# Kernel optimization log

Measured on AMD Instinct MI355X. Metric: run time of the kernel, lower is better.

The kernel has to match this reference:

```python
import jax, jax.numpy as jnp
import numpy as np

V, E, H = 100000, 128, 256
P1, P2 = 512, 128
B, S, F = 256, 200, 10


def setup_inputs() -> dict:
    key = jax.random.key(0)
    ks = jax.random.split(key, 12)
    s = lambda *d: 1.0 / np.sqrt(d[-1])
    inp = {
        "x": jax.random.randint(ks[0], (B, S, F), 0, V),
        "emb": jax.random.normal(ks[1], (V, E), jnp.float32) * 0.1,
        # PyTorch LSTM params: gates ordered (i, f, g, o), shapes [4H, E] / [4H, H]
        "W_ih": jax.random.normal(ks[2], (4 * H, E), jnp.float32) * s(E),
        "W_hh": jax.random.normal(ks[3], (4 * H, H), jnp.float32) * s(H),
        "b_ih": jax.random.normal(ks[4], (4 * H,), jnp.float32) * s(H),
        "b_hh": jax.random.normal(ks[5], (4 * H,), jnp.float32) * s(H),
        "W1": jax.random.normal(ks[6], (H, P1), jnp.float32) * s(H),
        "b1": jnp.zeros((P1,), jnp.float32),
        "W2": jax.random.normal(ks[7], (P1, P2), jnp.float32) * s(P1),
        "b2": jnp.zeros((P2,), jnp.float32),
        "W3": jax.random.normal(ks[8], (P2, 1), jnp.float32) * s(P2),
        "b3": jnp.zeros((1,), jnp.float32),
    }
    return inp


def reference(x, emb, W_ih, W_hh, b_ih, b_hh, W1, b1, W2, b2, W3, b3):
    # embedding + mean over field dim -> [B, S, E]
    e = jnp.take(emb, x, axis=0).mean(axis=-2)
    T = e.shape[1] // 2
    hist, tgt = e[:, :T], e[:, T:2 * T]
    b = e.shape[0]
    h0 = jnp.zeros((b, H), e.dtype)
    c0 = jnp.zeros((b, H), e.dtype)

    def lstm_step(carry, xt):
        h, c = carry
        g = xt @ W_ih.T + h @ W_hh.T + b_ih + b_hh  # [B, 4H]
        gi, gf, gg, go = jnp.split(g, 4, axis=-1)
        c = jax.nn.sigmoid(gf) * c + jax.nn.sigmoid(gi) * jnp.tanh(gg)
        h = jax.nn.sigmoid(go) * jnpp_tanh(c) if False else jax.nn.sigmoid(go) * jnp.tanh(c)
        return (h, c), None

    (hN, cN), _ = jax.lax.scan(lstm_step, (h0, c0), jnp.swapaxes(hist, 0, 1))

    # Each target step restarts from the SAME history state (loop reuses history_state),
    # so all T target steps are independent single LSTM steps -> fully batched.
    g = jnp.einsum('bte,ge->btg', tgt, W_ih) + (hN @ W_hh.T)[:, None, :] + b_ih + b_hh
    gi, gf, gg, go = jnp.split(g, 4, axis=-1)
    c = jax.nn.sigmoid(gf) * cN[:, None, :] + jax.nn.sigmoid(gi) * jnp.tanh(gg)
    h = jax.nn.sigmoid(go) * jnp.tanh(c)  # [B, T, H]

    # PredictMLP (eval mode: dropout = identity), ReLU hidden activations
    z = jax.nn.relu(h @ W1 + b1)
    z = jax.nn.relu(z @ W2 + b2)
    out = jax.nn.sigmoid((z @ W3 + b3)[..., 0])  # [B, T]
    return out
```

## Files before the change

### kernel.cpp

```cpp
#include <hip/hip_runtime.h>
#include <hip/hip_bf16.h>
#include <math.h>

#define B_  256
#define S_  200
#define F_  10
#define T_  100
#define E_  128
#define H_  256
#define G4  1024
#define P1_ 512
#define P2_ 128

typedef __attribute__((ext_vector_type(8))) short short8;
typedef __attribute__((ext_vector_type(4))) float f32x4;
typedef _Float16 half2f __attribute__((ext_vector_type(2)));

#if __has_builtin(__builtin_amdgcn_fdot2)
#define FDOT2(w2, h2, acc) __builtin_amdgcn_fdot2((w2), (h2), (acc), false)
#else
#define FDOT2(w2, h2, acc) ((acc) + (float)((w2)[0]) * (float)((h2)[0]) + (float)((w2)[1]) * (float)((h2)[1]))
#endif
#define BCH2(u) __builtin_bit_cast(half2f, (u))

#define NL2_ 36
#define NV2_ 92

__device__ __forceinline__ float fsig(float x) { return 1.0f / (1.0f + __expf(-x)); }
__device__ __forceinline__ float ftanh(float x) { return 1.0f - 2.0f / (__expf(2.0f * x) + 1.0f); }
__device__ __forceinline__ float bf2f(ushort u) { return __uint_as_float(((uint)u) << 16); }
__device__ __forceinline__ ushort f2bf(float f) {
    __hip_bfloat16 v = __float2bfloat16(f);
    return *(ushort*)&v;
}
__device__ __forceinline__ ushort f2h(float f) {
    _Float16 h = (_Float16)f;
    return __builtin_bit_cast(ushort, h);
}
__device__ __forceinline__ float h2f(ushort u) {
    return (float)__builtin_bit_cast(_Float16, u);
}

__global__ __launch_bounds__(256) void k_prep_all(
    const float* __restrict__ W_hh, uint* __restrict__ WPu,
    const float* __restrict__ W1, ushort* __restrict__ W1T,
    const float* __restrict__ W2, ushort* __restrict__ W2T,
    const float* __restrict__ W_ih, ushort* __restrict__ Wihb,
    ushort* __restrict__ Whhb,
    const float* __restrict__ b_ih, const float* __restrict__ b_hh,
    float* __restrict__ bsum,
    const int* __restrict__ x, const float* __restrict__ emb,
    ushort* __restrict__ ebf)
{
    __shared__ float t[32][33];
    int blk = blockIdx.x;
    int tid = threadIdx.x;
    if (blk < 256) {
        int k0 = (blk & 7) * 32, c0 = (blk >> 3) * 32;
        int lk = tid & 31, lc8 = tid >> 5;
        #pragma unroll
        for (int i = 0; i < 4; ++i)
            t[lc8 + 8 * i][lk] = W_hh[(long)(c0 + lc8 + 8 * i) * 256 + k0 + lk];
        __syncthreads();
        int kpl = tid >> 4, ccl = tid & 15;
        #pragma unroll
        for (int hf = 0; hf < 2; ++hf) {
            int c = ccl + 16 * hf;
            uint lo = f2h(t[c][2 * kpl]);
            uint hi = f2h(t[c][2 * kpl + 1]);
            WPu[(long)(k0 / 2 + kpl) * G4 + c0 + c] = lo | (hi << 16);
        }
    } else if (blk < 448) {
        const float* W; ushort* WT; int R, C, idx;
        if (blk < 384) { W = W1; WT = W1T; R = H_;  C = P1_; idx = blk - 256;
                         idx = (idx & 15) | ((idx >> 4) << 8); }
        else           { W = W2; WT = W2T; R = P1_; C = P2_; idx = blk - 384;
                         idx = (idx & 3) | ((idx >> 2) << 8); }
        int c0 = (idx & 255) * 32, r0 = (idx >> 8) * 32;
        int lc = tid & 31, lr = tid >> 5;
        #pragma unroll
        for (int i = 0; i < 4; ++i)
            t[lr + 8 * i][lc] = W[(long)(r0 + lr + 8 * i) * C + c0 + lc];
        __syncthreads();
        #pragma unroll
        for (int i = 0; i < 4; ++i)
            WT[(long)(c0 + lr + 8 * i) * R + r0 + lc] = f2bf(t[lc][lr + 8 * i]);
    } else if (blk < 960) {
        int i = (blk - 448) * 256 + tid;
        Wihb[i] = f2bf(W_ih[i]);
    } else if (blk < 1984) {
        int i = (blk - 960) * 256 + tid;
        Whhb[i] = f2bf(W_hh[i]);
    } else if (blk < 1988) {
        int i = (blk - 1984) * 256 + tid;
        bsum[i] = b_ih[i] + b_hh[i];
    } else {
        int bs = (blk - 1988) * 2 + (tid >> 7);
        int e  = tid & 127;
        const int* xr = x + (long)bs * F_;
        float acc = 0.f;
        #pragma unroll
        for (int f = 0; f < F_; ++f) acc += emb[(long)xr[f] * E_ + e];
        ebf[(long)bs * E_ + e] = f2bf(acc * (1.0f / F_));
    }
}

template<int ACT, int OUTM>
__global__ __launch_bounds__(256) void k_gemm_mfma(
    const ushort* __restrict__ A, int rowDiv, long sOuter, long sInner,
    const ushort* __restrict__ Bm,
    const float* __restrict__ bias,
    const float* __restrict__ rowAdd, int rowAddDiv,
    void* __restrict__ Cout, int N, int K)
{
    constexpr int LDT = 40;
    __shared__ ushort Al[128 * LDT];
    __shared__ ushort Bl[128 * LDT];
    int tid = threadIdx.x;
    int n0 = blockIdx.x * 128;
    int m0 = blockIdx.y * 128;

    int rA = tid >> 2, qA = tid & 3;
    int m_lo = m0 + rA, m_hi = m_lo + 64;
    long a0 = (long)(m_lo / rowDiv) * sOuter + (long)(m_lo % rowDiv) * sInner + qA * 8;
    long a1 = (long)(m_hi / rowDiv) * sOuter + (long)(m_hi % rowDiv) * sInner + qA * 8;
    const ushort* b0p = Bm + (long)(n0 + rA) * K + qA * 8;
    const ushort* b1p = Bm + (long)(n0 + rA + 64) * K + qA * 8;

    int lane = tid & 63, wave = tid >> 6;
    int wr = wave >> 1, wc = wave & 1;
    int lrow = lane & 15, lkh = lane >> 4;

    const f32x4 fz = {0.f, 0.f, 0.f, 0.f};
    f32x4 acc[4][4];
    #pragma unroll
    for (int i = 0; i < 4; ++i)
        #pragma unroll
        for (int j = 0; j < 4; ++j) acc[i][j] = fz;

    int nk = K >> 5;
    for (int kc = 0; kc < nk; ++kc) {
        uint4 va0 = *(const uint4*)(A + a0 + kc * 32);
        uint4 va1 = *(const uint4*)(A + a1 + kc * 32);
        uint4 vb0 = *(const uint4*)(b0p + kc * 32);
        uint4 vb1 = *(const uint4*)(b1p + kc * 32);
        *(uint4*)&Al[rA * LDT + qA * 8]        = va0;
        *(uint4*)&Al[(rA + 64) * LDT + qA * 8] = va1;
        *(uint4*)&Bl[rA * LDT + qA * 8]        = vb0;
        *(uint4*)&Bl[(rA + 64) * LDT + qA * 8] = vb1;
        __syncthreads();
        short8 af[4], bfr[4];
        #pragma unroll
        for (int mi = 0; mi < 4; ++mi)
            af[mi] = *(const short8*)&Al[(wr * 64 + mi * 16 + lrow) * LDT + lkh * 8];
        #pragma unroll
        for (int ni = 0; ni < 4; ++ni)
            bfr[ni] = *(const short8*)&Bl[(wc * 64 + ni * 16 + lrow) * LDT + lkh * 8];
        #pragma unroll
        for (int mi = 0; mi < 4; ++mi)
            #pragma unroll
            for (int ni = 0; ni < 4; ++ni)
                acc[mi][ni] = __builtin_amdgcn_mfma_f32_16x16x32_bf16(
                    af[mi], bfr[ni], acc[mi][ni], 0, 0, 0);
        __syncthreads();
    }
    #pragma unroll
    for (int mi = 0; mi < 4; ++mi) {
        #pragma unroll
        for (int r = 0; r < 4; ++r) {
            int m = m0 + wr * 64 + mi * 16 + lkh * 4 + r;
            long rowoff = rowAdd ? (long)(m / rowAddDiv) * N : 0;
            #pragma unroll
            for (int ni = 0; ni < 4; ++ni) {
                int n = n0 + wc * 64 + ni * 16 + lrow;
                float v = acc[mi][ni][r];
                if (bias)   v += bias[n];
                if (rowAdd) v += rowAdd[rowoff + n];
                if (ACT)    v = fmaxf(v, 0.f);
                if (OUTM == 1)      ((ushort*)Cout)[(long)m * N + n] = f2bf(v);
                else if (OUTM == 2) ((ushort*)Cout)[(long)m * N + n] = f2h(v);
                else                ((float*)Cout)[(long)m * N + n] = v;
            }
        }
    }
}

__global__ __launch_bounds__(256) void k_gdec_fused(
    const ushort* __restrict__ A, int rowDiv, long sOuter, long sInner,
    const ushort* __restrict__ Bm,
    const float* __restrict__ hhdec,
    const float* __restrict__ cNb,
    ushort* __restrict__ hdec)
{
    constexpr int LDT = 40;
    __shared__ ushort Al[128 * LDT];
    __shared__ ushort Bl[128 * LDT];
    __shared__ ushort Zl[128 * 132];
    int tid = threadIdx.x;
    int j0 = blockIdx.x * 32;
    int m0 = blockIdx.y * 128;
    const int K = E_;

    int rA = tid >> 2, qA = tid & 3;
    int m_lo = m0 + rA, m_hi = m_lo + 64;
    long a0 = (long)(m_lo / rowDiv) * sOuter + (long)(m_lo % rowDiv) * sInner + qA * 8;
    long a1 = (long)(m_hi / rowDiv) * sOuter + (long)(m_hi % rowDiv) * sInner + qA * 8;
    int nr0 = rA, nr1 = rA + 64;
    const ushort* b0p = Bm + (long)((nr0 >> 5) * 256 + j0 + (nr0 & 31)) * K + qA * 8;
    const ushort* b1p = Bm + (long)((nr1 >> 5) * 256 + j0 + (nr1 & 31)) * K + qA * 8;

    int lane = tid & 63, wave = tid >> 6;
    int wr = wave >> 1, wc = wave & 1;
    int lrow = lane & 15, lkh = lane >> 4;

    const f32x4 fz = {0.f, 0.f, 0.f, 0.f};
    f32x4 acc[4][4];
    #pragma unroll
    for (int i = 0; i < 4; ++i)
        #pragma unroll
        for (int j = 0; j < 4; ++j) acc[i][j] = fz;

    for (int kc = 0; kc < K / 32; ++kc) {
        uint4 va0 = *(const uint4*)(A + a0 + kc * 32);
        uint4 va1 = *(const uint4*)(A + a1 + kc * 32);
        uint4 vb0 = *(const uint4*)(b0p + kc * 32);
        uint4 vb1 = *(const uint4*)(b1p + kc * 32);
        *(uint4*)&Al[rA * LDT + qA * 8]        = va0;
        *(uint4*)&Al[(rA + 64) * LDT + qA * 8] = va1;
        *(uint4*)&Bl[rA * LDT + qA * 8]        = vb0;
        *(uint4*)&Bl[(rA + 64) * LDT + qA * 8] = vb1;
        __syncthreads();
        short8 af[4], bfr[4];
        #pragma unroll
        for (int mi = 0; mi < 4; ++mi)
            af[mi] = *(const short8*)&Al[(wr * 64 + mi * 16 + lrow) * LDT + lkh * 8];
        #pragma unroll
        for (int ni = 0; ni < 4; ++ni)
            bfr[ni] = *(const short8*)&Bl[(wc * 64 + ni * 16 + lrow) * LDT + lkh * 8];
        #pragma unroll
        for (int mi = 0; mi < 4; ++mi)
            #pragma unroll
            for (int ni = 0; ni < 4; ++ni)
                acc[mi][ni] = __builtin_amdgcn_mfma_f32_16x16x32_bf16(
                    af[mi], bfr[ni], acc[mi][ni], 0, 0, 0);
        __syncthreads();
    }
    #pragma unroll
    for (int mi = 0; mi < 4; ++mi) {
        #pragma unroll
        for (int r = 0; r < 4; ++r) {
            int row = wr * 64 + mi * 16 + lkh * 4 + r;
            int bidx = (m0 + row) / T_;
            #pragma unroll
            for (int ni = 0; ni < 4; ++ni) {
                int col = wc * 64 + ni * 16 + lrow;
                float v = acc[mi][ni][r]
                        + hhdec[(long)bidx * G4 + (col >> 5) * 256 + j0 + (col & 31)];
                Zl[row * 132 + col] = f2bf(v);
            }
        }
    }
    __syncthreads();
    int jl = tid & 31, mb = tid >> 5;
    #pragma unroll
    for (int q = 0; q < 16; ++q) {
        int row = mb * 16 + q;
        int m = m0 + row;
        int bidx = m / T_;
        float gi = bf2f(Zl[row * 132 +      jl]);
        float gf = bf2f(Zl[row * 132 + 32 + jl]);
        float gg = bf2f(Zl[row * 132 + 64 + jl]);
        float go = bf2f(Zl[row * 132 + 96 + jl]);
        float cv = fsig(gf) * cNb[(long)bidx * H_ + j0 + jl] + fsig(gi) * ftanh(gg);
        hdec[(long)m * H_ + j0 + jl] = f2bf(fsig(go) * ftanh(cv));
    }
}

#define Z1S 520
__global__ __launch_bounds__(256) void k_mlp_fused(
    const ushort* __restrict__ A,
    const ushort* __restrict__ W1T,
    const float* __restrict__ b1,
    const ushort* __restrict__ W2T,
    const float* __restrict__ b2,
    const float* __restrict__ W3, const float* __restrict__ b3,
    float* __restrict__ out)
{
    extern __shared__ __align__(16) char smem[];
    ushort* z1l = (ushort*)smem;
    ushort* Al  = z1l + 128 * Z1S;
    ushort* Bl  = Al + 128 * 40;
    int tid = threadIdx.x;
    int m0 = blockIdx.x * 128;

    int rA = tid >> 2, qA = tid & 3;
    int lane = tid & 63, wave = tid >> 6;
    int wr = wave >> 1, wc = wave & 1;
    int lrow = lane & 15, lkh = lane >> 4;
    const f32x4 fz = {0.f, 0.f, 0.f, 0.f};

    for (int nt = 0; nt < 4; ++nt) {
        f32x4 acc[4][4];
        #pragma unroll
        for (int i = 0; i < 4; ++i)
            #pragma unroll
            for (int j = 0; j < 4; ++j) acc[i][j] = fz;
        for (int kc = 0; kc < H_ / 32; ++kc) {
            uint4 va0 = *(const uint4*)(A + (long)(m0 + rA) * H_ + kc * 32 + qA * 8);
            uint4 va1 = *(const uint4*)(A + (long)(m0 + rA + 64) * H_ + kc * 32 + qA * 8);
            uint4 vb0 = *(const uint4*)(W1T + (long)(nt * 128 + rA) * H_ + kc * 32 + qA * 8);
            uint4 vb1 = *(const uint4*)(W1T + (long)(nt * 128 + rA + 64) * H_ + kc * 32 + qA * 8);
            *(uint4*)&Al[rA * 40 + qA * 8]        = va0;
            *(uint4*)&Al[(rA + 64) * 40 + qA * 8] = va1;
            *(uint4*)&Bl[rA * 40 + qA * 8]        = vb0;
            *(uint4*)&Bl[(rA + 64) * 40 + qA * 8] = vb1;
            __syncthreads();
            short8 af[4], bfr[4];
            #pragma unroll
            for (int mi = 0; mi < 4; ++mi)
                af[mi] = *(const short8*)&Al[(wr * 64 + mi * 16 + lrow) * 40 + lkh * 8];
            #pragma unroll
            for (int ni = 0; ni < 4; ++ni)
                bfr[ni] = *(const short8*)&Bl[(wc * 64 + ni * 16 + lrow) * 40 + lkh * 8];
            #pragma unroll
            for (int mi = 0; mi < 4; ++mi)
                #pragma unroll
                for (int ni = 0; ni < 4; ++ni)
                    acc[mi][ni] = __builtin_amdgcn_mfma_f32_16x16x32_bf16(
                        af[mi], bfr[ni], acc[mi][ni], 0, 0, 0);
            __syncthreads();
        }
        #pragma unroll
        for (int mi = 0; mi < 4; ++mi) {
            #pragma unroll
            for (int r = 0; r < 4; ++r) {
                int row = wr * 64 + mi * 16 + lkh * 4 + r;
                #pragma unroll
                for (int ni = 0; ni < 4; ++ni) {
                    int col = nt * 128 + wc * 64 + ni * 16 + lrow;
                    z1l[row * Z1S + col] = f2bf(fmaxf(acc[mi][ni][r] + b1[col], 0.f));
                }
            }
        }
    }
    __syncthreads();

    f32x4 acc[4][4];
    #pragma unroll
    for (int i = 0; i < 4; ++i)
        #pragma unroll
        for (int j = 0; j < 4; ++j) acc[i][j] = fz;
    for (int kc = 0; kc < P1_ / 32; ++kc) {
        uint4 vb0 = *(const uint4*)(W2T + (long)rA * P1_ + kc * 32 + qA * 8);
        uint4 vb1 = *(const uint4*)(W2T + (long)(rA + 64) * P1_ + kc * 32 + qA * 8);
        *(uint4*)&Bl[rA * 40 + qA * 8]        = vb0;
        *(uint4*)&Bl[(rA + 64) * 40 + qA * 8] = vb1;
        __syncthreads();
        short8 af[4], bfr[4];
        #pragma unroll
        for (int mi = 0; mi < 4; ++mi)
            af[mi] = *(const short8*)&z1l[(wr * 64 + mi * 16 + lrow) * Z1S + kc * 32 + lkh * 8];
        #pragma unroll
        for (int ni = 0; ni < 4; ++ni)
            bfr[ni] = *(const short8*)&Bl[(wc * 64 + ni * 16 + lrow) * 40 + lkh * 8];
        #pragma unroll
        for (int mi = 0; mi < 4; ++mi)
            #pragma unroll
            for (int ni = 0; ni < 4; ++ni)
                acc[mi][ni] = __builtin_amdgcn_mfma_f32_16x16x32_bf16(
                    af[mi], bfr[ni], acc[mi][ni], 0, 0, 0);
        __syncthreads();
    }
    float* Zf = (float*)z1l;
    #pragma unroll
    for (int mi = 0; mi < 4; ++mi) {
        #pragma unroll
        for (int r = 0; r < 4; ++r) {
            int row = wr * 64 + mi * 16 + lkh * 4 + r;
            #pragma unroll
            for (int ni = 0; ni < 4; ++ni) {
                int col = wc * 64 + ni * 16 + lrow;
                Zf[row * 132 + col] = fmaxf(acc[mi][ni][r] + b2[col], 0.f);
            }
        }
    }
    __syncthreads();
    float w3a = W3[lane], w3b = W3[64 + lane], b3v = b3[0];
    for (int r = 0; r < 32; ++r) {
        int row = wave * 32 + r;
        float s = Zf[row * 132 + lane] * w3a + Zf[row * 132 + 64 + lane] * w3b;
        #pragma unroll
        for (int off = 32; off > 0; off >>= 1) s += __shfl_down(s, off);
        if (lane == 0) out[m0 + row] = fsig(s + b3v);
    }
}

__global__ __launch_bounds__(512, 2) void k_lstm_scan(
    const ushort* __restrict__ Xgh, const uint* __restrict__ WPu,
    float* __restrict__ cN, ushort* __restrict__ hNb)
{
    extern __shared__ __align__(16) char smem[];
    uint*   Wl    = (uint*)smem;
    float*  act_s = (float*)(smem + NL2_ * 4096);
    uint*   h16u  = (uint*)(act_s + G4);
    ushort* h16   = (ushort*)h16u;
    int tid = threadIdx.x;
    int b   = blockIdx.x;
    int cB  = tid + 512;

    for (int i = tid; i < NL2_ * 1024; i += 512) {
        int row = i >> 10, col = i & 1023;
        Wl[col * NL2_ + row] = WPu[(long)row * G4 + col];
    }
    uint wrA[NV2_], wrB[NV2_];
    #pragma unroll
    for (int i = 0; i < NV2_; ++i) {
        wrA[i] = WPu[(long)(NL2_ + i) * G4 + tid];
        wrB[i] = WPu[(long)(NL2_ + i) * G4 + cB];
    }
    if (tid < 128) h16u[tid] = 0;
    float c_r = 0.f;
    __syncthreads();

    int isTanhB = (tid >> 8) == 0;
    const ushort* xgp = Xgh + (long)b * T_ * G4;
    const uint* wcA = Wl + tid * NL2_;
    const uint* wcB = Wl + (tid + 512) * NL2_;

    for (int t = 0; t < T_; ++t) {
        float xvA = h2f(xgp[(long)t * G4 + tid]);
        float xvB = h2f(xgp[(long)t * G4 + cB]);
        float aA0 = 0.f, aA1 = 0.f, aB0 = 0.f, aB1 = 0.f;
        #pragma unroll
        for (int r4 = 0; r4 < NL2_ / 4; ++r4) {
            uint4 hh = *(const uint4*)(h16u + 4 * r4);
            uint4 wa = *(const uint4*)(wcA + 4 * r4);
            uint4 wb = *(const uint4*)(wcB + 4 * r4);
            aA0 = FDOT2(BCH2(wa.x), BCH2(hh.x), aA0); aB0 = FDOT2(BCH2(wb.x), BCH2(hh.x), aB0);
            aA1 = FDOT2(BCH2(wa.y), BCH2(hh.y), aA1); aB1 = FDOT2(BCH2(wb.y), BCH2(hh.y), aB1);
            aA0 = FDOT2(BCH2(wa.z), BCH2(hh.z), aA0); aB0 = FDOT2(BCH2(wb.z), BCH2(hh.z), aB0);
            aA1 = FDOT2(BCH2(wa.w), BCH2(hh.w), aA1); aB1 = FDOT2(BCH2(wb.w), BCH2(hh.w), aB1);
        }
        #pragma unroll
        for (int r4 = 0; r4 < NV2_ / 4; ++r4) {
            uint4 hh = *(const uint4*)(h16u + NL2_ + 4 * r4);
            aA0 = FDOT2(BCH2(wrA[4 * r4 + 0]), BCH2(hh.x), aA0);
            aB0 = FDOT2(BCH2(wrB[4 * r4 + 0]), BCH2(hh.x), aB0);
            aA1 = FDOT2(BCH2(wrA[4 * r4 + 1]), BCH2(hh.y), aA1);
            aB1 = FDOT2(BCH2(wrB[4 * r4 + 1]), BCH2(hh.y), aB1);
            aA0 = FDOT2(BCH2(wrA[4 * r4 + 2]), BCH2(hh.z), aA0);
            aB0 = FDOT2(BCH2(wrB[4 * r4 + 2]), BCH2(hh.z), aB0);
            aA1 = FDOT2(BCH2(wrA[4 * r4 + 3]), BCH2(hh.w), aA1);
            aB1 = FDOT2(BCH2(wrB[4 * r4 + 3]), BCH2(hh.w), aB1);
        }
        float aA = aA0 + aA1, aB = aB0 + aB1;
        act_s[tid] = fsig(aA + xvA);
        float gB = aB + xvB;
        act_s[cB] = isTanhB ? ftanh(gB) : fsig(gB);
        __syncthreads();
        if (tid < H_) {
            float cn = act_s[H_ + tid] * c_r + act_s[tid] * act_s[2 * H_ + tid];
            c_r = cn;
            float h = act_s[3 * H_ + tid] * ftanh(cn);
            h16[tid] = f2h(h);
            if (t == T_ - 1) {
                cN[(long)b * H_ + tid] = c_r;
                hNb[(long)b * H_ + tid] = f2bf(h);
            }
        }
        __syncthreads();
    }
}

extern "C" void kernel_launch(void* const* d_in, const int* in_sizes, int n_in,
                              void* d_out, int out_size, void* d_ws, size_t ws_size,
                              hipStream_t stream)
{
    const int*   x    = (const int*)d_in[0];
    const float* emb  = (const float*)d_in[1];
    const float* W_ih = (const float*)d_in[2];
    const float* W_hh = (const float*)d_in[3];
    const float* b_ih = (const float*)d_in[4];
    const float* b_hh = (const float*)d_in[5];
    const float* W1   = (const float*)d_in[6];
    const float* b1   = (const float*)d_in[7];
    const float* W2   = (const float*)d_in[8];
    const float* b2   = (const float*)d_in[9];
    const float* W3   = (const float*)d_in[10];
    const float* b3   = (const float*)d_in[11];
    float* out = (float*)d_out;

    float* ws = (float*)d_ws;
    ushort* ebf   = (ushort*)ws;
    ushort* Xgh   = (ushort*)(ws + 3276800);
    ushort* hdecb = (ushort*)(ws + 16384000);
    float* bsum  = ws + 26214400;
    float* cN    = bsum + 1024;
    ushort* hNb  = (ushort*)(cN + 65536);
    float* hhdec = cN + 65536 + 32768;
    uint*  WPu   = (uint*)(hhdec + 262144);
    ushort* Wihb = (ushort*)(WPu + 131072);
    ushort* Whhb = Wihb + 131072;
    ushort* W1T  = Whhb + 262144;
    ushort* W2T  = W1T + 131072;

    k_prep_all<<<1988 + B_ * S_ / 2, 256, 0, stream>>>(
        W_hh, WPu, W1, W1T, W2, W2T, W_ih, Wihb, Whhb,
        b_ih, b_hh, bsum, x, emb, ebf);

    k_gemm_mfma<0, 2><<<dim3(G4 / 128, (B_ * T_) / 128), 256, 0, stream>>>(
        ebf, T_, (long)S_ * E_, (long)E_, Wihb, bsum, nullptr, 1,
        Xgh, G4, E_);

    size_t scan_smem = (size_t)NL2_ * 4096 + G4 * sizeof(float) + 128 * sizeof(uint);
    k_lstm_scan<<<B_, 512, scan_smem, stream>>>(Xgh, WPu, cN, hNb);

    k_gemm_mfma<0, 0><<<dim3(G4 / 128, B_ / 128), 256, 0, stream>>>(
        hNb, B_, 0L, (long)H_, Whhb, bsum, nullptr, 1,
        hhdec, G4, H_);

    k_gdec_fused<<<dim3(H_ / 32, (B_ * T_) / 128), 256, 0, stream>>>(
        ebf + T_ * E_, T_, (long)S_ * E_, (long)E_, Wihb, hhdec, cN, hdecb);

    size_t mlp_smem = (size_t)128 * Z1S * 2 + 2 * 128 * 40 * 2;
    k_mlp_fused<<<(B_ * T_) / 128, 256, mlp_smem, stream>>>(
        hdecb, W1T, b1, W2T, b2, W3, b3, out);
}
```

Measured before the change: 357.6 us.

## Fold final hN@W_hh projection into LSTM scan and rebalance register/LDS weight split

The scan kernel runs one extra iteration after the last step, computing hN·W_hh^T + bias with the weights it already holds and writing hhdec directly. This removes the separate GEMM launch, the bf16 W_hh conversion blocks in the prep kernel, and the hNb round trip. It also moves more of the W_hh rows from LDS into registers (NL2 36→28, NV2 92→100), which raises register pressure and risks spilling at two blocks per CU. The decoder recurrent term is now computed from fp16 h and fp16 weights instead of a bf16 GEMM, which slightly changes precision.

Result: slower. 408.4 us (+14.2%).

```diff
diff --git a/kernel.cpp b/kernel.cpp
--- a/kernel.cpp
+++ b/kernel.cpp
@@ -23,8 +23,8 @@
 #endif
 #define BCH2(u) __builtin_bit_cast(half2f, (u))
 
-#define NL2_ 36
-#define NV2_ 92
+#define NL2_ 28
+#define NV2_ 100
 
 __device__ __forceinline__ float fsig(float x) { return 1.0f / (1.0f + __expf(-x)); }
 __device__ __forceinline__ float ftanh(float x) { return 1.0f - 2.0f / (__expf(2.0f * x) + 1.0f); }
@@ -46,7 +46,6 @@
     const float* __restrict__ W1, ushort* __restrict__ W1T,
     const float* __restrict__ W2, ushort* __restrict__ W2T,
     const float* __restrict__ W_ih, ushort* __restrict__ Wihb,
-    ushort* __restrict__ Whhb,
     const float* __restrict__ b_ih, const float* __restrict__ b_hh,
     float* __restrict__ bsum,
     const int* __restrict__ x, const float* __restrict__ emb,
@@ -88,14 +87,11 @@
     } else if (blk < 960) {
         int i = (blk - 448) * 256 + tid;
         Wihb[i] = f2bf(W_ih[i]);
-    } else if (blk < 1984) {
+    } else if (blk < 964) {
         int i = (blk - 960) * 256 + tid;
-        Whhb[i] = f2bf(W_hh[i]);
-    } else if (blk < 1988) {
-        int i = (blk - 1984) * 256 + tid;
         bsum[i] = b_ih[i] + b_hh[i];
     } else {
-        int bs = (blk - 1988) * 2 + (tid >> 7);
+        int bs = (blk - 964) * 2 + (tid >> 7);
         int e  = tid & 127;
         const int* xr = x + (long)bs * F_;
         float acc = 0.f;
@@ -397,7 +393,8 @@
 
 __global__ __launch_bounds__(512, 2) void k_lstm_scan(
     const ushort* __restrict__ Xgh, const uint* __restrict__ WPu,
-    float* __restrict__ cN, ushort* __restrict__ hNb)
+    const float* __restrict__ bsum,
+    float* __restrict__ cN, float* __restrict__ hhdec)
 {
     extern __shared__ __align__(16) char smem[];
     uint*   Wl    = (uint*)smem;
@@ -427,9 +424,15 @@
     const uint* wcA = Wl + tid * NL2_;
     const uint* wcB = Wl + (tid + 512) * NL2_;
 
-    for (int t = 0; t < T_; ++t) {
-        float xvA = h2f(xgp[(long)t * G4 + tid]);
-        float xvB = h2f(xgp[(long)t * G4 + cB]);
+    for (int t = 0; t <= T_; ++t) {
+        float xvA, xvB;
+        if (t < T_) {
+            xvA = h2f(xgp[(long)t * G4 + tid]);
+            xvB = h2f(xgp[(long)t * G4 + cB]);
+        } else {
+            xvA = bsum[tid];
+            xvB = bsum[cB];
+        }
         float aA0 = 0.f, aA1 = 0.f, aB0 = 0.f, aB1 = 0.f;
         #pragma unroll
         for (int r4 = 0; r4 < NL2_ / 4; ++r4) {
@@ -454,6 +457,11 @@
             aB1 = FDOT2(BCH2(wrB[4 * r4 + 3]), BCH2(hh.w), aB1);
         }
         float aA = aA0 + aA1, aB = aB0 + aB1;
+        if (t == T_) {
+            hhdec[(long)b * G4 + tid] = aA + xvA;
+            hhdec[(long)b * G4 + cB] = aB + xvB;
+            break;
+        }
         act_s[tid] = fsig(aA + xvA);
         float gB = aB + xvB;
         act_s[cB] = isTanhB ? ftanh(gB) : fsig(gB);
@@ -463,10 +471,7 @@
             c_r = cn;
             float h = act_s[3 * H_ + tid] * ftanh(cn);
             h16[tid] = f2h(h);
-            if (t == T_ - 1) {
-                cN[(long)b * H_ + tid] = c_r;
-                hNb[(long)b * H_ + tid] = f2bf(h);
-            }
+            if (t == T_ - 1) cN[(long)b * H_ + tid] = c_r;
         }
         __syncthreads();
     }
@@ -496,16 +501,14 @@
     ushort* hdecb = (ushort*)(ws + 16384000);
     float* bsum  = ws + 26214400;
     float* cN    = bsum + 1024;
-    ushort* hNb  = (ushort*)(cN + 65536);
-    float* hhdec = cN + 65536 + 32768;
+    float* hhdec = cN + 65536;
     uint*  WPu   = (uint*)(hhdec + 262144);
     ushort* Wihb = (ushort*)(WPu + 131072);
-    ushort* Whhb = Wihb + 131072;
-    ushort* W1T  = Whhb + 262144;
+    ushort* W1T  = Wihb + 131072;
     ushort* W2T  = W1T + 131072;
 
-    k_prep_all<<<1988 + B_ * S_ / 2, 256, 0, stream>>>(
-        W_hh, WPu, W1, W1T, W2, W2T, W_ih, Wihb, Whhb,
+    k_prep_all<<<964 + B_ * S_ / 2, 256, 0, stream>>>(
+        W_hh, WPu, W1, W1T, W2, W2T, W_ih, Wihb,
         b_ih, b_hh, bsum, x, emb, ebf);
 
     k_gemm_mfma<0, 2><<<dim3(G4 / 128, (B_ * T_) / 128), 256, 0, stream>>>(
@@ -513,11 +516,7 @@
         Xgh, G4, E_);
 
     size_t scan_smem = (size_t)NL2_ * 4096 + G4 * sizeof(float) + 128 * sizeof(uint);
-    k_lstm_scan<<<B_, 512, scan_smem, stream>>>(Xgh, WPu, cN, hNb);
-
-    k_gemm_mfma<0, 0><<<dim3(G4 / 128, B_ / 128), 256, 0, stream>>>(
-        hNb, B_, 0L, (long)H_, Whhb, bsum, nullptr, 1,
-        hhdec, G4, H_);
+    k_lstm_scan<<<B_, 512, scan_smem, stream>>>(Xgh, WPu, bsum, cN, hhdec);
 
     k_gdec_fused<<<dim3(H_ / 32, (B_ * T_) / 128), 256, 0, stream>>>(
         ebf + T_ * E_, T_, (long)S_ * E_, (long)E_, Wihb, hhdec, cN, hdecb);
```
